# Performance work log

Measured on AMD Instinct MI355X. Metric: run time of the kernel, lower is better.

## Reference

```python
import jax, jax.numpy as jnp
import numpy as np
import math

SCALES = [1, 2, 4, 8]
H = 1024           # hidden_size
NS = len(SCALES)
DS = H // NS       # per-scale dim = 256
NH_S = max(1, 8 // NS)  # heads per scale = 2


def _avg_pool(x, s):
    # x: [B, L, d], kernel=stride=s (L divisible by s)
    B, L, d = x.shape
    return x.reshape(B, L // s, s, d).mean(axis=2)


def _mha(q, k, v, in_w, in_b, out_w, out_b, nh):
    # torch nn.MultiheadAttention, batch_first, no mask.
    d = q.shape[-1]
    wq, wk, wv = in_w[:d], in_w[d:2 * d], in_w[2 * d:]
    bq, bk, bv = in_b[:d], in_b[d:2 * d], in_b[2 * d:]
    qh = q @ wq.T + bq
    kh = k @ wk.T + bk
    vh = v @ wv.T + bv
    B, Lq, _ = qh.shape
    Lk = kh.shape[1]
    hd = d // nh
    qh = qh.reshape(B, Lq, nh, hd).transpose(0, 2, 1, 3)
    kh = kh.reshape(B, Lk, nh, hd).transpose(0, 2, 1, 3)
    vh = vh.reshape(B, Lk, nh, hd).transpose(0, 2, 1, 3)
    scores = jnp.einsum('bhqd,bhkd->bhqk', qh, kh) * (1.0 / math.sqrt(hd))
    w = jax.nn.softmax(scores, axis=-1)
    out = jnp.einsum('bhqk,bhkd->bhqd', w, vh)
    out = out.transpose(0, 2, 1, 3).reshape(B, Lq, d)
    out = out @ out_w.T + out_b
    return out, w.mean(axis=1)  # averaged attn weights (torch default)


def setup_inputs() -> dict:
    key = jax.random.key(0)
    ks = jax.random.split(key, 20)
    B, S = 4, 2048
    f = lambda k, shape: (jax.random.normal(k, shape, dtype=jnp.float32) * 0.02)
    return {
        'query': jax.random.normal(ks[0], (B, S, H), dtype=jnp.float32),
        'key': jax.random.normal(ks[1], (B, S, H), dtype=jnp.float32),
        'value': jax.random.normal(ks[2], (B, S, H), dtype=jnp.float32),
        'wq': f(ks[3], (H, H)), 'bq': f(ks[4], (H,)),
        'wk': f(ks[5], (H, H)), 'bk': f(ks[6], (H,)),
        'wv': f(ks[7], (H, H)), 'bv': f(ks[8], (H,)),
        'mha_in_w': f(ks[9], (NS, 3 * DS, DS)),
        'mha_in_b': f(ks[10], (NS, 3 * DS)),
        'mha_out_w': f(ks[11], (NS, DS, DS)),
        'mha_out_b': f(ks[12], (NS, DS)),
        'fus_w': f(ks[13], (H, H)), 'fus_b': f(ks[14], (H,)),
    }


def reference(query, key, value, wq, bq, wk, bk, wv, bv,
              mha_in_w, mha_in_b, mha_out_w, mha_out_b, fus_w, fus_b):
    q = query @ wq.T + bq
    k = key @ wk.T + bk
    v = value @ wv.T + bv
    outs = []
    weights0 = None
    for i, s in enumerate(SCALES):
        qs = q[..., i * DS:(i + 1) * DS]
        ks_ = k[..., i * DS:(i + 1) * DS]
        vs = v[..., i * DS:(i + 1) * DS]
        if s > 1:
            ks_ = _avg_pool(ks_, s)
            vs = _avg_pool(vs, s)
        attended, w = _mha(qs, ks_, vs, mha_in_w[i], mha_in_b[i],
                           mha_out_w[i], mha_out_b[i], NH_S)
        # F.interpolate back to seq_len is an identity here (query length == seq_len)
        outs.append(attended)
        if i == 0:
            weights0 = w
    fused = jnp.concatenate(outs, axis=-1) @ fus_w.T + fus_b
    return fused, weights0
```

## Files before the change

kernel.cpp:

```cpp
#include <hip/hip_runtime.h>
#include <stdint.h>

typedef unsigned short u16;
typedef __bf16 v8bf __attribute__((ext_vector_type(8)));
typedef float v4f __attribute__((ext_vector_type(4)));
typedef __attribute__((address_space(3))) unsigned lds_t;
typedef const __attribute__((address_space(1))) unsigned g_t;

__device__ __forceinline__ u16 f2bf(float f) {
  union { float f; unsigned u; } v; v.f = f;
  unsigned r = v.u + 0x7FFFu + ((v.u >> 16) & 1u);
  return (u16)(r >> 16);
}
__device__ __forceinline__ float bf2f(u16 h) {
  union { unsigned u; float f; } v; v.u = ((unsigned)h) << 16;
  return v.f;
}
__device__ __forceinline__ ushort4 f4bf(float4 f) {
  ushort4 o;
  o.x = f2bf(f.x); o.y = f2bf(f.y); o.z = f2bf(f.z); o.w = f2bf(f.w);
  return o;
}

__global__ void k_cvt(const float* __restrict__ s, u16* __restrict__ d, long n) {
  long i = ((long)blockIdx.x * blockDim.x + threadIdx.x) * 4;
  long stride = (long)gridDim.x * blockDim.x * 4;
  for (; i < n; i += stride) {
    *(ushort4*)(d + i) = f4bf(*(const float4*)(s + i));
  }
}

__global__ void k_cvtpool(const float* __restrict__ src, u16* __restrict__ dst) {
  int g = blockIdx.x & 255, b = blockIdx.x >> 8;
  int c = threadIdx.x * 4;
  const float* p = src + ((long)b * 2048 + g * 8) * 1024 + c;
  u16* df = dst + ((long)b * 2048 + g * 8) * 1024 + c;
  float4 x[8];
#pragma unroll
  for (int j = 0; j < 8; j++) {
    x[j] = *(const float4*)(p + (long)j * 1024);
    *(ushort4*)(df + (long)j * 1024) = f4bf(x[j]);
  }
  float4 s2[4], s4[2], s8;
#pragma unroll
  for (int j = 0; j < 4; j++) {
    s2[j].x = x[2 * j].x + x[2 * j + 1].x;
    s2[j].y = x[2 * j].y + x[2 * j + 1].y;
    s2[j].z = x[2 * j].z + x[2 * j + 1].z;
    s2[j].w = x[2 * j].w + x[2 * j + 1].w;
  }
#pragma unroll
  for (int j = 0; j < 2; j++) {
    s4[j].x = s2[2 * j].x + s2[2 * j + 1].x;
    s4[j].y = s2[2 * j].y + s2[2 * j + 1].y;
    s4[j].z = s2[2 * j].z + s2[2 * j + 1].z;
    s4[j].w = s2[2 * j].w + s2[2 * j + 1].w;
  }
  s8.x = s4[0].x + s4[1].x; s8.y = s4[0].y + s4[1].y;
  s8.z = s4[0].z + s4[1].z; s8.w = s4[0].w + s4[1].w;
  u16* d2 = dst + ((long)8192 + b * 1024 + g * 4) * 1024 + c;
#pragma unroll
  for (int j = 0; j < 4; j++) {
    float4 t = {s2[j].x * 0.5f, s2[j].y * 0.5f, s2[j].z * 0.5f, s2[j].w * 0.5f};
    *(ushort4*)(d2 + (long)j * 1024) = f4bf(t);
  }
  u16* d4 = dst + ((long)12288 + b * 512 + g * 2) * 1024 + c;
#pragma unroll
  for (int j = 0; j < 2; j++) {
    float4 t = {s4[j].x * 0.25f, s4[j].y * 0.25f, s4[j].z * 0.25f, s4[j].w * 0.25f};
    *(ushort4*)(d4 + (long)j * 1024) = f4bf(t);
  }
  float4 t8 = {s8.x * 0.125f, s8.y * 0.125f, s8.z * 0.125f, s8.w * 0.125f};
  *(ushort4*)(dst + ((long)14336 + b * 256 + g) * 1024 + c) = f4bf(t8);
}

__global__ void k_tc(const float* __restrict__ src, u16* __restrict__ dst, int R, int C) {
  __shared__ float t[32][33];
  long zoff = (long)blockIdx.z * R * C;
  int r0 = blockIdx.y * 32, c0 = blockIdx.x * 32;
  int tx = threadIdx.x & 31, ty = threadIdx.x >> 5;
#pragma unroll
  for (int j = 0; j < 32; j += 8)
    t[ty + j][tx] = src[zoff + (long)(r0 + ty + j) * C + c0 + tx];
  __syncthreads();
#pragma unroll
  for (int j = 0; j < 32; j += 8)
    dst[zoff + (long)(c0 + ty + j) * R + r0 + tx] = f2bf(t[tx][ty + j]);
}

__global__ void k_bcomb_qkv(const float* __restrict__ in_w, const float* __restrict__ in_b,
                            const float* __restrict__ bq, const float* __restrict__ bk,
                            const float* __restrict__ bv, float* __restrict__ out) {
  int gw = (blockIdx.x * 256 + threadIdx.x) >> 6;
  int lane = threadIdx.x & 63;
  int p = gw >> 10, j = gw & 1023, i = j >> 8, of = j & 255;
  const float* bp = p == 0 ? bq : p == 1 ? bk : bv;
  const float* row = in_w + ((long)i * 768 + p * 256 + of) * 256;
  float s = 0.f;
#pragma unroll
  for (int m = 0; m < 4; m++) s += row[lane + m * 64] * bp[i * 256 + lane + m * 64];
#pragma unroll
  for (int m = 32; m >= 1; m >>= 1) s += __shfl_xor(s, m, 64);
  if (lane == 0) out[gw] = in_b[(long)i * 768 + p * 256 + of] + s;
}

__global__ void k_bcomb_f(const float* __restrict__ fw, const float* __restrict__ fb,
                          const float* __restrict__ ob, float* __restrict__ out) {
  int w = (blockIdx.x * 256 + threadIdx.x) >> 6;
  int lane = threadIdx.x & 63;
  const float* row = fw + (long)w * 1024;
  float s = 0.f;
  for (int k = lane; k < 1024; k += 64) s += row[k] * ob[k];
#pragma unroll
  for (int m = 32; m >= 1; m >>= 1) s += __shfl_xor(s, m, 64);
  if (lane == 0) out[w] = fb[w] + s;
}

template<int KS>
__global__ __launch_bounds__(256) void k_ksum(const float* __restrict__ P,
                                              u16* __restrict__ O, long n, int coloff) {
  long i = ((long)blockIdx.x * 256 + threadIdx.x) * 4;
  if (i >= n) return;
  float4 s = *(const float4*)(P + i);
#pragma unroll
  for (int ks = 1; ks < KS; ks++) {
    float4 t = *(const float4*)(P + (long)ks * n + i);
    s.x += t.x; s.y += t.y; s.z += t.z; s.w += t.w;
  }
  *(ushort4*)(O + (i >> 8) * 1024 + coloff + (int)(i & 255)) = f4bf(s);
}

__global__ __launch_bounds__(256) void k_ml0(
    const u16* __restrict__ QHf, const u16* __restrict__ KH,
    float* __restrict__ Mp, float* __restrict__ Lp)
{
  int kc = blockIdx.x;
  int z = blockIdx.z;
  int b = z >> 1, h = z & 1;
  int q0 = blockIdx.y * 64;
  __shared__ u16 KV[2][128][32];
  __shared__ float red[2][4][64];

  const int tid = threadIdx.x, lane = tid & 63, wave = tid >> 6;
  const int q4 = lane >> 4, l16 = lane & 15;
  const int wr = (wave >> 1) * 32, wc = (wave & 1) * 64;
  const int srow = wave * 16 + (lane >> 2), scol = (lane & 3) * 8;
  const float alpha = 0.08838834764831845f;

  v8bf qf[2][4];
#pragma unroll
  for (int mi = 0; mi < 2; mi++)
#pragma unroll
    for (int sub = 0; sub < 4; sub++)
      qf[mi][sub] = *(const v8bf*)(QHf + ((long)b * 2048 + q0 + wr + mi * 16 + l16) * 1024
                                   + h * 128 + sub * 32 + q4 * 8);

  const u16* gK = KH + (long)b * 2048 * 256 + h * 128;
  auto stageK = [&](int buf, int kt, int sub) {
    const u16* g = gK + (long)(kt * 128 + srow) * 256 + sub * 32 + scol;
    __builtin_amdgcn_global_load_lds((g_t*)g, (lds_t*)&KV[buf][wave * 16][0], 16, 0, 0);
    __builtin_amdgcn_global_load_lds((g_t*)(g + 64 * 256), (lds_t*)&KV[buf][64 + wave * 16][0], 16, 0, 0);
  };

  float m_run[2][4], l_run[2][4];
#pragma unroll
  for (int mi = 0; mi < 2; mi++)
#pragma unroll
    for (int i4 = 0; i4 < 4; i4++) { m_run[mi][i4] = -1e30f; l_run[mi][i4] = 0.f; }

  for (int kt = kc * 4; kt < kc * 4 + 4; kt++) {
    v4f s[2][4];
#pragma unroll
    for (int mi = 0; mi < 2; mi++)
#pragma unroll
      for (int ni = 0; ni < 4; ni++) s[mi][ni] = (v4f){0.f, 0.f, 0.f, 0.f};
    stageK(0, kt, 0);
    __syncthreads();
    int cur = 0;
#pragma unroll
    for (int sub = 0; sub < 4; sub++) {
      if (sub < 3) stageK(cur ^ 1, kt, sub + 1);
      v8bf kf[4];
#pragma unroll
      for (int ni = 0; ni < 4; ni++)
        kf[ni] = *(const v8bf*)&KV[cur][wc + ni * 16 + l16][q4 * 8];
#pragma unroll
      for (int mi = 0; mi < 2; mi++)
#pragma unroll
        for (int ni = 0; ni < 4; ni++)
          s[mi][ni] = __builtin_amdgcn_mfma_f32_16x16x32_bf16(qf[mi][sub], kf[ni], s[mi][ni], 0, 0, 0);
      __syncthreads();
      cur ^= 1;
    }
#pragma unroll
    for (int mi = 0; mi < 2; mi++)
#pragma unroll
      for (int ni = 0; ni < 4; ni++) s[mi][ni] *= alpha;
    float mloc[2][4];
#pragma unroll
    for (int mi = 0; mi < 2; mi++)
#pragma unroll
      for (int i4 = 0; i4 < 4; i4++)
        mloc[mi][i4] = fmaxf(fmaxf(s[mi][0][i4], s[mi][1][i4]),
                             fmaxf(s[mi][2][i4], s[mi][3][i4]));
#pragma unroll
    for (int d = 1; d <= 8; d <<= 1)
#pragma unroll
      for (int mi = 0; mi < 2; mi++)
#pragma unroll
        for (int i4 = 0; i4 < 4; i4++)
          mloc[mi][i4] = fmaxf(mloc[mi][i4], __shfl_xor(mloc[mi][i4], d, 64));
    if (l16 == 0) {
#pragma unroll
      for (int mi = 0; mi < 2; mi++)
#pragma unroll
        for (int i4 = 0; i4 < 4; i4++)
          red[0][wave][wr + mi * 16 + q4 * 4 + i4] = mloc[mi][i4];
    }
    __syncthreads();
    float lloc[2][4] = {{0.f, 0.f, 0.f, 0.f}, {0.f, 0.f, 0.f, 0.f}};
#pragma unroll
    for (int mi = 0; mi < 2; mi++)
#pragma unroll
      for (int i4 = 0; i4 < 4; i4++) {
        int rr = wr + mi * 16 + q4 * 4 + i4;
        float mn = fmaxf(fmaxf(red[0][wave][rr], red[0][wave ^ 1][rr]), m_run[mi][i4]);
        float scl = __expf(m_run[mi][i4] - mn);
        m_run[mi][i4] = mn;
        l_run[mi][i4] *= scl;
#pragma unroll
        for (int ni = 0; ni < 4; ni++)
          lloc[mi][i4] += __expf(s[mi][ni][i4] - mn);
      }
#pragma unroll
    for (int d = 1; d <= 8; d <<= 1)
#pragma unroll
      for (int mi = 0; mi < 2; mi++)
#pragma unroll
        for (int i4 = 0; i4 < 4; i4++)
          lloc[mi][i4] += __shfl_xor(lloc[mi][i4], d, 64);
    if (l16 == 0) {
#pragma unroll
      for (int mi = 0; mi < 2; mi++)
#pragma unroll
        for (int i4 = 0; i4 < 4; i4++)
          red[1][wave][wr + mi * 16 + q4 * 4 + i4] = lloc[mi][i4];
    }
    __syncthreads();
#pragma unroll
    for (int mi = 0; mi < 2; mi++)
#pragma unroll
      for (int i4 = 0; i4 < 4; i4++) {
        int rr = wr + mi * 16 + q4 * 4 + i4;
        l_run[mi][i4] += red[1][wave][rr] + red[1][wave ^ 1][rr];
      }
    __syncthreads();
  }

  if ((wave & 1) == 0 && l16 == 0) {
    long zo = ((long)kc * 8 + z) * 2048;
#pragma unroll
    for (int mi = 0; mi < 2; mi++)
#pragma unroll
      for (int i4 = 0; i4 < 4; i4++) {
        int r = q0 + wr + mi * 16 + q4 * 4 + i4;
        Mp[zo + r] = m_run[mi][i4];
        Lp[zo + r] = l_run[mi][i4];
      }
  }
}

__global__ __launch_bounds__(256) void k_mlcomb(
    const float* __restrict__ Mp, const float* __restrict__ Lp,
    float* __restrict__ M0, float* __restrict__ L0)
{
  long r = (long)blockIdx.x * 256 + threadIdx.x;
  float m = -1e30f;
#pragma unroll
  for (int kc = 0; kc < 4; kc++) m = fmaxf(m, Mp[kc * 16384 + r]);
  float l = 0.f;
#pragma unroll
  for (int kc = 0; kc < 4; kc++)
    l += Lp[kc * 16384 + r] * __expf(Mp[kc * 16384 + r] - m);
  M0[r] = m; L0[r] = l;
}

__global__ __launch_bounds__(256) void k_pv0(
    const u16* __restrict__ QHf, const u16* __restrict__ KH,
    const u16* __restrict__ VHT, const float* __restrict__ M0,
    const float* __restrict__ L0, float* __restrict__ PP, float* __restrict__ W0)
{
  int kc = blockIdx.x;
  int b = blockIdx.z;
  int q0 = blockIdx.y * 32;
  __shared__ u16 P[2][32][136];
  __shared__ u16 KV[2][128][32];

  const int tid = threadIdx.x, lane = tid & 63, wave = tid >> 6;
  const int q4 = lane >> 4, l16 = lane & 15;
  const int wr = (wave >> 1) * 16, wc = (wave & 1) * 64;
  const int srow = wave * 16 + (lane >> 2), scol = (lane & 3) * 8;
  const float alpha = 0.08838834764831845f;

  v8bf qf[2][4];
#pragma unroll
  for (int h = 0; h < 2; h++)
#pragma unroll
    for (int sub = 0; sub < 4; sub++)
      qf[h][sub] = *(const v8bf*)(QHf + ((long)b * 2048 + q0 + wr + l16) * 1024
                                  + h * 128 + sub * 32 + q4 * 8);
  float mv[2][4], il[2][4];
#pragma unroll
  for (int h = 0; h < 2; h++)
#pragma unroll
    for (int i4 = 0; i4 < 4; i4++) {
      long r = (long)(b * 2 + h) * 2048 + q0 + wr + q4 * 4 + i4;
      mv[h][i4] = M0[r];
      il[h][i4] = 1.0f / L0[r];
    }

  const u16* gK = KH + (long)b * 2048 * 256;
  auto stageK = [&](int buf, int h, int kt, int sub) {
    const u16* g = gK + (long)(kt * 128 + srow) * 256 + h * 128 + sub * 32 + scol;
    __builtin_amdgcn_global_load_lds((g_t*)g, (lds_t*)&KV[buf][wave * 16][0], 16, 0, 0);
    __builtin_amdgcn_global_load_lds((g_t*)(g + 64 * 256), (lds_t*)&KV[buf][64 + wave * 16][0], 16, 0, 0);
  };
  auto stageV = [&](int buf, int h, int kt, int sub) {
    const u16* g = VHT + ((long)(b * 2 + h) * 128 + srow) * 2048 + kt * 128 + sub * 32 + scol;
    __builtin_amdgcn_global_load_lds((g_t*)g, (lds_t*)&KV[buf][wave * 16][0], 16, 0, 0);
    __builtin_amdgcn_global_load_lds((g_t*)(g + (long)64 * 2048), (lds_t*)&KV[buf][64 + wave * 16][0], 16, 0, 0);
  };

  v4f acc[2][4];
#pragma unroll
  for (int h = 0; h < 2; h++)
#pragma unroll
    for (int ni = 0; ni < 4; ni++) acc[h][ni] = (v4f){0.f, 0.f, 0.f, 0.f};

  for (int kt = kc * 4; kt < kc * 4 + 4; kt++) {
    float p0[4][4];
#pragma unroll
    for (int h = 0; h < 2; h++) {
      v4f s[4];
#pragma unroll
      for (int ni = 0; ni < 4; ni++) s[ni] = (v4f){0.f, 0.f, 0.f, 0.f};
      stageK(0, h, kt, 0);
      __syncthreads();
      int cur = 0;
#pragma unroll
      for (int sub = 0; sub < 4; sub++) {
        if (sub < 3) stageK(cur ^ 1, h, kt, sub + 1);
        v8bf kf[4];
#pragma unroll
        for (int ni = 0; ni < 4; ni++)
          kf[ni] = *(const v8bf*)&KV[cur][wc + ni * 16 + l16][q4 * 8];
#pragma unroll
        for (int ni = 0; ni < 4; ni++)
          s[ni] = __builtin_amdgcn_mfma_f32_16x16x32_bf16(qf[h][sub], kf[ni], s[ni], 0, 0, 0);
        __syncthreads();
        cur ^= 1;
      }
#pragma unroll
      for (int ni = 0; ni < 4; ni++)
#pragma unroll
        for (int i4 = 0; i4 < 4; i4++) {
          float p = __expf(s[ni][i4] * alpha - mv[h][i4]) * il[h][i4];
          P[h][wr + q4 * 4 + i4][wc + ni * 16 + l16] = f2bf(p);
          if (h == 0) p0[ni][i4] = p;
          else {
            W0[((long)b * 2048 + q0 + wr + q4 * 4 + i4) * 2048
               + kt * 128 + wc + ni * 16 + l16] = 0.5f * (p0[ni][i4] + p);
          }
        }
    }
#pragma unroll
    for (int h = 0; h < 2; h++) {
      stageV(0, h, kt, 0);
      __syncthreads();
      int cv = 0;
#pragma unroll
      for (int sub = 0; sub < 4; sub++) {
        if (sub < 3) stageV(cv ^ 1, h, kt, sub + 1);
        v8bf pf = *(const v8bf*)&P[h][wr + l16][sub * 32 + q4 * 8];
        v8bf vf[4];
#pragma unroll
        for (int ni = 0; ni < 4; ni++)
          vf[ni] = *(const v8bf*)&KV[cv][wc + ni * 16 + l16][q4 * 8];
#pragma unroll
        for (int ni = 0; ni < 4; ni++)
          acc[h][ni] = __builtin_amdgcn_mfma_f32_16x16x32_bf16(pf, vf[ni], acc[h][ni], 0, 0, 0);
        __syncthreads();
        cv ^= 1;
      }
    }
  }

  float* pp = PP + ((long)kc * 8192 + (long)b * 2048) * 256;
#pragma unroll
  for (int h = 0; h < 2; h++)
#pragma unroll
    for (int ni = 0; ni < 4; ni++)
#pragma unroll
      for (int i4 = 0; i4 < 4; i4++) {
        int r = q0 + wr + q4 * 4 + i4;
        int c = wc + ni * 16 + l16;
        pp[(long)r * 256 + h * 128 + c] = acc[h][ni][i4];
      }
}

__global__ __launch_bounds__(256) void k_flash(
    const u16* __restrict__ QHf, const u16* __restrict__ KH,
    const u16* __restrict__ VHT, u16* __restrict__ AOf)
{
  int z = blockIdx.z;
  int i = (z >> 3) + 1;
  int b = (z >> 1) & 3, h = z & 1;
  int Ls = 2048 >> i;
  int nkt = Ls >> 7;
  long ro = (long)(16384 - (8192 >> (i - 1))) * 256;
  int q0 = blockIdx.y * 64;

  __shared__ u16 QP[64][136];
  __shared__ u16 KV[2][128][32];
  __shared__ float red[2][4][64];

  const int tid = threadIdx.x, lane = tid & 63, wave = tid >> 6;
  const int q4 = lane >> 4, l16 = lane & 15;
  const int wr = (wave >> 1) * 32, wc = (wave & 1) * 64;
  const int srow = wave * 16 + (lane >> 2);
  const int scol = (lane & 3) * 8;

  {
    const u16* gq = QHf + ((long)b * 2048 + q0) * 1024 + i * 256 + h * 128;
    int idx = tid * 4;
#pragma unroll
    for (int j = 0; j < 4; j++) {
      int r = (idx + j) >> 4, ch = (idx + j) & 15;
      *(ulonglong2*)&QP[r][ch * 8] = *(const ulonglong2*)(gq + (long)r * 1024 + ch * 8);
    }
  }
  __syncthreads();
  v8bf qf[2][4];
#pragma unroll
  for (int mi = 0; mi < 2; mi++)
#pragma unroll
    for (int sub = 0; sub < 4; sub++)
      qf[mi][sub] = *(const v8bf*)&QP[wr + mi * 16 + l16][sub * 32 + q4 * 8];
  __syncthreads();

  const u16* gK = KH + ro + (long)b * Ls * 256 + h * 128;
  const u16* gV = VHT + ro + (long)(b * 2 + h) * 128 * Ls;

  auto stageK = [&](int buf, int kt, int sub) {
    const u16* g = gK + (long)(kt * 128 + srow) * 256 + sub * 32 + scol;
    __builtin_amdgcn_global_load_lds((g_t*)g, (lds_t*)&KV[buf][wave * 16][0], 16, 0, 0);
    __builtin_amdgcn_global_load_lds((g_t*)(g + 64 * 256), (lds_t*)&KV[buf][64 + wave * 16][0], 16, 0, 0);
  };
  auto stageV = [&](int buf, int kt, int sub) {
    const u16* g = gV + (long)srow * Ls + kt * 128 + sub * 32 + scol;
    __builtin_amdgcn_global_load_lds((g_t*)g, (lds_t*)&KV[buf][wave * 16][0], 16, 0, 0);
    __builtin_amdgcn_global_load_lds((g_t*)(g + (long)64 * Ls), (lds_t*)&KV[buf][64 + wave * 16][0], 16, 0, 0);
  };

  v4f acc_o[2][4];
  float m_run[2][4], l_run[2][4];
#pragma unroll
  for (int mi = 0; mi < 2; mi++)
#pragma unroll
    for (int ni = 0; ni < 4; ni++) acc_o[mi][ni] = (v4f){0.f, 0.f, 0.f, 0.f};
#pragma unroll
  for (int mi = 0; mi < 2; mi++)
#pragma unroll
    for (int i4 = 0; i4 < 4; i4++) { m_run[mi][i4] = -1e30f; l_run[mi][i4] = 0.f; }

  const float alpha = 0.08838834764831845f;

  for (int kt = 0; kt < nkt; kt++) {
    v4f s[2][4];
#pragma unroll
    for (int mi = 0; mi < 2; mi++)
#pragma unroll
      for (int ni = 0; ni < 4; ni++) s[mi][ni] = (v4f){0.f, 0.f, 0.f, 0.f};
    stageK(0, kt, 0);
    __syncthreads();
    int cur = 0;
#pragma unroll
    for (int sub = 0; sub < 4; sub++) {
      if (sub < 3) stageK(cur ^ 1, kt, sub + 1);
      v8bf kf[4];
#pragma unroll
      for (int ni = 0; ni < 4; ni++)
        kf[ni] = *(const v8bf*)&KV[cur][wc + ni * 16 + l16][q4 * 8];
#pragma unroll
      for (int mi = 0; mi < 2; mi++)
#pragma unroll
        for (int ni = 0; ni < 4; ni++)
          s[mi][ni] = __builtin_amdgcn_mfma_f32_16x16x32_bf16(qf[mi][sub], kf[ni], s[mi][ni], 0, 0, 0);
      __syncthreads();
      cur ^= 1;
    }
    stageV(0, kt, 0);

#pragma unroll
    for (int mi = 0; mi < 2; mi++)
#pragma unroll
      for (int ni = 0; ni < 4; ni++) s[mi][ni] *= alpha;
    float mloc[2][4];
#pragma unroll
    for (int mi = 0; mi < 2; mi++)
#pragma unroll
      for (int i4 = 0; i4 < 4; i4++)
        mloc[mi][i4] = fmaxf(fmaxf(s[mi][0][i4], s[mi][1][i4]),
                             fmaxf(s[mi][2][i4], s[mi][3][i4]));
#pragma unroll
    for (int d = 1; d <= 8; d <<= 1)
#pragma unroll
      for (int mi = 0; mi < 2; mi++)
#pragma unroll
        for (int i4 = 0; i4 < 4; i4++)
          mloc[mi][i4] = fmaxf(mloc[mi][i4], __shfl_xor(mloc[mi][i4], d, 64));
    if (l16 == 0) {
#pragma unroll
      for (int mi = 0; mi < 2; mi++)
#pragma unroll
        for (int i4 = 0; i4 < 4; i4++)
          red[0][wave][wr + mi * 16 + q4 * 4 + i4] = mloc[mi][i4];
    }
    __syncthreads();
    float scl[2][4];
#pragma unroll
    for (int mi = 0; mi < 2; mi++)
#pragma unroll
      for (int i4 = 0; i4 < 4; i4++) {
        int rr = wr + mi * 16 + q4 * 4 + i4;
        float mn = fmaxf(fmaxf(red[0][wave][rr], red[0][wave ^ 1][rr]), m_run[mi][i4]);
        scl[mi][i4] = __expf(m_run[mi][i4] - mn);
        m_run[mi][i4] = mn;
      }
    float lloc[2][4] = {{0.f, 0.f, 0.f, 0.f}, {0.f, 0.f, 0.f, 0.f}};
#pragma unroll
    for (int mi = 0; mi < 2; mi++)
#pragma unroll
      for (int ni = 0; ni < 4; ni++)
#pragma unroll
        for (int i4 = 0; i4 < 4; i4++) {
          float p = __expf(s[mi][ni][i4] - m_run[mi][i4]);
          lloc[mi][i4] += p;
          QP[wr + mi * 16 + q4 * 4 + i4][wc + ni * 16 + l16] = f2bf(p);
        }
#pragma unroll
    for (int d = 1; d <= 8; d <<= 1)
#pragma unroll
      for (int mi = 0; mi < 2; mi++)
#pragma unroll
        for (int i4 = 0; i4 < 4; i4++)
          lloc[mi][i4] += __shfl_xor(lloc[mi][i4], d, 64);
    if (l16 == 0) {
#pragma unroll
      for (int mi = 0; mi < 2; mi++)
#pragma unroll
        for (int i4 = 0; i4 < 4; i4++)
          red[1][wave][wr + mi * 16 + q4 * 4 + i4] = lloc[mi][i4];
    }
#pragma unroll
    for (int mi = 0; mi < 2; mi++)
#pragma unroll
      for (int ni = 0; ni < 4; ni++)
#pragma unroll
        for (int i4 = 0; i4 < 4; i4++) acc_o[mi][ni][i4] *= scl[mi][i4];
    __syncthreads();
#pragma unroll
    for (int mi = 0; mi < 2; mi++)
#pragma unroll
      for (int i4 = 0; i4 < 4; i4++) {
        int rr = wr + mi * 16 + q4 * 4 + i4;
        l_run[mi][i4] = l_run[mi][i4] * scl[mi][i4] + red[1][wave][rr] + red[1][wave ^ 1][rr];
      }

    int cv = 0;
#pragma unroll
    for (int sub = 0; sub < 4; sub++) {
      if (sub < 3) stageV(cv ^ 1, kt, sub + 1);
      v8bf pf[2], vf[4];
#pragma unroll
      for (int mi = 0; mi < 2; mi++)
        pf[mi] = *(const v8bf*)&QP[wr + mi * 16 + l16][sub * 32 + q4 * 8];
#pragma unroll
      for (int ni = 0; ni < 4; ni++)
        vf[ni] = *(const v8bf*)&KV[cv][wc + ni * 16 + l16][q4 * 8];
#pragma unroll
      for (int mi = 0; mi < 2; mi++)
#pragma unroll
        for (int ni = 0; ni < 4; ni++)
          acc_o[mi][ni] = __builtin_amdgcn_mfma_f32_16x16x32_bf16(pf[mi], vf[ni], acc_o[mi][ni], 0, 0, 0);
      __syncthreads();
      cv ^= 1;
    }
  }

#pragma unroll
  for (int mi = 0; mi < 2; mi++)
#pragma unroll
    for (int i4 = 0; i4 < 4; i4++) {
      float inv = 1.0f / l_run[mi][i4];
#pragma unroll
      for (int ni = 0; ni < 4; ni++) {
        int r = q0 + wr + mi * 16 + q4 * 4 + i4;
        int c = wc + ni * 16 + l16;
        AOf[((long)b * 2048 + r) * 1024 + i * 256 + h * 128 + c] =
            f2bf(acc_o[mi][ni][i4] * inv);
      }
    }
}

template<int WBF>
__global__ __launch_bounds__(256) void k_gemm(
    const u16* __restrict__ A, long ldA, long sA1, long sA2,
    const u16* __restrict__ B, long ldB, long sB1, long sB2,
    void* __restrict__ Cv, long ldC, long sC1, long sC2, long sCk,
    const float* __restrict__ bias, long sBias, float alpha,
    int M, int N, int K, int nz2, int KS)
{
  __shared__ u16 As[2][128][32];
  __shared__ u16 Bs[2][128][32];
  int z = blockIdx.z;
  int ks = z % KS; int zz = z / KS;
  int z1 = zz / nz2, z2 = zz - z1 * nz2;
  A += (long)z1 * sA1 + (long)z2 * sA2 + (long)ks * K;
  B += (long)z1 * sB1 + (long)z2 * sB2 + (long)ks * K;
  long coff = (long)z1 * sC1 + (long)z2 * sC2 + (long)ks * sCk;
  const float* bz = bias ? bias + (long)z2 * sBias : nullptr;
  const int m0 = blockIdx.y * 128, n0 = blockIdx.x * 128;
  const int tid = threadIdx.x;
  const int lane = tid & 63;
  const int wave = tid >> 6;
  const int wr = (wave >> 1) * 64, wc = (wave & 1) * 64;
  const int q4 = lane >> 4, l16 = lane & 15;

  const int srow = wave * 16 + (lane >> 2);
  const int scol = (lane & 3) * 8;
  const u16* gA = A + (long)(m0 + srow) * ldA + scol;
  const u16* gB = B + (long)(n0 + srow) * ldB + scol;

  auto stage = [&](int buf, int kt) {
    __builtin_amdgcn_global_load_lds((g_t*)(gA + kt), (lds_t*)&As[buf][wave * 16][0], 16, 0, 0);
    __builtin_amdgcn_global_load_lds((g_t*)(gA + 64 * ldA + kt), (lds_t*)&As[buf][64 + wave * 16][0], 16, 0, 0);
    __builtin_amdgcn_global_load_lds((g_t*)(gB + kt), (lds_t*)&Bs[buf][wave * 16][0], 16, 0, 0);
    __builtin_amdgcn_global_load_lds((g_t*)(gB + 64 * ldB + kt), (lds_t*)&Bs[buf][64 + wave * 16][0], 16, 0, 0);
  };

  v4f acc[4][4];
#pragma unroll
  for (int i = 0; i < 4; i++)
#pragma unroll
    for (int j = 0; j < 4; j++) acc[i][j] = (v4f){0.f, 0.f, 0.f, 0.f};

  stage(0, 0);
  __syncthreads();
  int cur = 0;
  for (int kt = 0; kt < K; kt += 32) {
    if (kt + 32 < K) stage(cur ^ 1, kt + 32);
    v8bf af[4], bf[4];
#pragma unroll
    for (int i = 0; i < 4; i++) af[i] = *(const v8bf*)&As[cur][wr + i * 16 + l16][q4 * 8];
#pragma unroll
    for (int i = 0; i < 4; i++) bf[i] = *(const v8bf*)&Bs[cur][wc + i * 16 + l16][q4 * 8];
#pragma unroll
    for (int mi = 0; mi < 4; mi++)
#pragma unroll
      for (int ni = 0; ni < 4; ni++)
        acc[mi][ni] = __builtin_amdgcn_mfma_f32_16x16x32_bf16(af[mi], bf[ni], acc[mi][ni], 0, 0, 0);
    __syncthreads();
    cur ^= 1;
  }

#pragma unroll
  for (int mi = 0; mi < 4; mi++) {
    int rb = m0 + wr + mi * 16 + q4 * 4;
#pragma unroll
    for (int ni = 0; ni < 4; ni++) {
      int c = n0 + wc + ni * 16 + l16;
      float bv = bz ? bz[c] : 0.f;
#pragma unroll
      for (int i = 0; i < 4; i++) {
        int r = rb + i;
        float val = acc[mi][ni][i] * alpha + bv;
        if (WBF) ((u16*)Cv)[coff + (long)r * ldC + c] = f2bf(val);
        else     ((float*)Cv)[coff + (long)r * ldC + c] = val;
      }
    }
  }
}

__global__ __launch_bounds__(256) void k_gemm_kv(
    const u16* __restrict__ Xk, const u16* __restrict__ Xv,
    const u16* __restrict__ WCkv, const float* __restrict__ Bckv,
    u16* __restrict__ KH, u16* __restrict__ VHT)
{
  __shared__ u16 As[2][128][32];
  __shared__ u16 Bs[2][128][32];
  const int isV = blockIdx.z;
  const int m0 = blockIdx.y * 128, n0 = blockIdx.x * 128;
  const int scale = m0 < 8192 ? 0 : (m0 < 12288 ? 1 : (m0 < 14336 ? 2 : 3));
  const int rbase = scale == 0 ? 0 : (scale == 1 ? 8192 : (scale == 2 ? 12288 : 14336));
  const int lsh = 11 - scale;
  const u16* A = isV ? Xv : Xk;
  const u16* B = WCkv + (long)isV * 1048576 + (long)scale * 262144;
  const float* bz = Bckv + isV * 1024 + scale * 256;

  const int tid = threadIdx.x;
  const int lane = tid & 63, wave = tid >> 6;
  const int wr = (wave >> 1) * 64, wc = (wave & 1) * 64;
  const int q4 = lane >> 4, l16 = lane & 15;
  const int srow = wave * 16 + (lane >> 2);
  const int scol = (lane & 3) * 8;
  const u16* gA = A + (long)(m0 + srow) * 1024 + scol;
  const u16* gB = B + (long)(n0 + srow) * 1024 + scol;

  auto stage = [&](int buf, int kt) {
    __builtin_amdgcn_global_load_lds((g_t*)(gA + kt), (lds_t*)&As[buf][wave * 16][0], 16, 0, 0);
    __builtin_amdgcn_global_load_lds((g_t*)(gA + 64 * 1024 + kt), (lds_t*)&As[buf][64 + wave * 16][0], 16, 0, 0);
    __builtin_amdgcn_global_load_lds((g_t*)(gB + kt), (lds_t*)&Bs[buf][wave * 16][0], 16, 0, 0);
    __builtin_amdgcn_global_load_lds((g_t*)(gB + 64 * 1024 + kt), (lds_t*)&Bs[buf][64 + wave * 16][0], 16, 0, 0);
  };

  v4f acc[4][4];
#pragma unroll
  for (int i = 0; i < 4; i++)
#pragma unroll
    for (int j = 0; j < 4; j++) acc[i][j] = (v4f){0.f, 0.f, 0.f, 0.f};

  stage(0, 0);
  __syncthreads();
  int cur = 0;
  for (int kt = 0; kt < 1024; kt += 32) {
    if (kt + 32 < 1024) stage(cur ^ 1, kt + 32);
    v8bf af[4], bf[4];
#pragma unroll
    for (int i = 0; i < 4; i++) af[i] = *(const v8bf*)&As[cur][wr + i * 16 + l16][q4 * 8];
#pragma unroll
    for (int i = 0; i < 4; i++) bf[i] = *(const v8bf*)&Bs[cur][wc + i * 16 + l16][q4 * 8];
#pragma unroll
    for (int mi = 0; mi < 4; mi++)
#pragma unroll
      for (int ni = 0; ni < 4; ni++)
        acc[mi][ni] = __builtin_amdgcn_mfma_f32_16x16x32_bf16(af[mi], bf[ni], acc[mi][ni], 0, 0, 0);
    __syncthreads();
    cur ^= 1;
  }

#pragma unroll
  for (int mi = 0; mi < 4; mi++) {
    int rb = m0 + wr + mi * 16 + q4 * 4;
#pragma unroll
    for (int ni = 0; ni < 4; ni++) {
      int c = n0 + wc + ni * 16 + l16;
      float bv = bz[c];
#pragma unroll
      for (int i = 0; i < 4; i++) {
        int r = rb + i;
        float val = acc[mi][ni][i] + bv;
        if (!isV) {
          KH[(long)r * 256 + c] = f2bf(val);
        } else {
          int rl = r - rbase;
          int b = rl >> lsh, t = rl & ((1 << lsh) - 1);
          int h = c >> 7, n = c & 127;
          VHT[(long)rbase * 256 + (((long)(b * 2 + h) * 128 + n) << lsh) + t] = f2bf(val);
        }
      }
    }
  }
}

extern "C" void kernel_launch(void* const* d_in, const int* in_sizes, int n_in,
                              void* d_out, int out_size, void* d_ws, size_t ws_size,
                              hipStream_t stream) {
  const float* query = (const float*)d_in[0];
  const float* key_  = (const float*)d_in[1];
  const float* value = (const float*)d_in[2];
  const float* wq    = (const float*)d_in[3];
  const float* bq    = (const float*)d_in[4];
  const float* wk    = (const float*)d_in[5];
  const float* bk    = (const float*)d_in[6];
  const float* wv    = (const float*)d_in[7];
  const float* bv    = (const float*)d_in[8];
  const float* in_w  = (const float*)d_in[9];
  const float* in_b  = (const float*)d_in[10];
  const float* out_w = (const float*)d_in[11];
  const float* out_b = (const float*)d_in[12];
  const float* fus_w = (const float*)d_in[13];
  const float* fus_b = (const float*)d_in[14];
  (void)in_sizes; (void)n_in; (void)out_size; (void)ws_size;

  float* outF  = (float*)d_out;
  float* outW0 = outF + (long)4 * 2048 * 1024;

  char* base = (char*)d_ws;
  size_t off = 0;
  auto alloc = [&](size_t bytes) -> void* {
    void* p = base + off;
    off = (off + bytes + 255) & ~(size_t)255;
    return p;
  };
  const long NX = (long)8192 * 1024;
  u16* Winb = (u16*)alloc((size_t)4 * 768 * 256 * 2);
  u16* Wfb  = (u16*)alloc((size_t)1024 * 1024 * 2);
  u16* WoT  = (u16*)alloc((size_t)4 * 256 * 256 * 2);
  u16* WT   = (u16*)alloc((size_t)3 * 1024 * 1024 * 2);
  u16* WC   = (u16*)alloc((size_t)3 * 1024 * 1024 * 2);
  u16* WFc  = (u16*)alloc((size_t)1024 * 1024 * 2);
  float* Bc  = (float*)alloc((size_t)3 * 1024 * 4);
  float* fbc = (float*)alloc((size_t)1024 * 4);
  u16* Xq    = (u16*)alloc((size_t)NX * 2);
  u16* XkAll = (u16*)alloc((size_t)15360 * 1024 * 2);
  u16* XvAll = (u16*)alloc((size_t)15360 * 1024 * 2);
  u16* QHf = (u16*)alloc((size_t)8192 * 1024 * 2);
  u16* KH  = (u16*)alloc((size_t)15360 * 256 * 2);
  u16* VHT = (u16*)alloc((size_t)15360 * 256 * 2);
  float* M0 = (float*)alloc((size_t)8 * 2048 * 4);
  float* L0 = (float*)alloc((size_t)8 * 2048 * 4);
  float* Mp = (float*)alloc((size_t)4 * 8 * 2048 * 4);
  float* Lp = (float*)alloc((size_t)4 * 8 * 2048 * 4);
  float* PP = (float*)alloc((size_t)4 * 8192 * 256 * 4);
  u16* AOf = (u16*)alloc((size_t)8192 * 1024 * 2);

  const long AOsz = (long)8192 * 256;

  k_cvt<<<1024, 256, 0, stream>>>(query, Xq, NX);
  k_cvtpool<<<1024, 256, 0, stream>>>(key_,  XkAll);
  k_cvtpool<<<1024, 256, 0, stream>>>(value, XvAll);
  k_cvt<<<192, 256, 0, stream>>>(in_w, Winb, 4 * 768 * 256);
  k_cvt<<<256, 256, 0, stream>>>(fus_w, Wfb, 1024 * 1024);
  k_tc<<<dim3(32, 32, 1), 256, 0, stream>>>(wq, WT, 1024, 1024);
  k_tc<<<dim3(32, 32, 1), 256, 0, stream>>>(wk, WT + (long)1024 * 1024, 1024, 1024);
  k_tc<<<dim3(32, 32, 1), 256, 0, stream>>>(wv, WT + (long)2 * 1024 * 1024, 1024, 1024);
  k_tc<<<dim3(8, 8, 4), 256, 0, stream>>>(out_w, WoT, 256, 256);
  k_bcomb_qkv<<<768, 256, 0, stream>>>(in_w, in_b, bq, bk, bv, Bc);
  k_bcomb_f<<<256, 256, 0, stream>>>(fus_w, fus_b, out_b, fbc);

  k_gemm<1><<<dim3(8, 2, 12), 256, 0, stream>>>(
      Winb, 256, 65536, 196608,
      WT, 1024, 1048576, 256,
      WC, 1024, 1048576, 262144, 0,
      nullptr, 0, 1.f, 256, 1024, 256, 4, 1);
  k_gemm<1><<<dim3(2, 8, 4), 256, 0, stream>>>(
      Wfb, 1024, 0, 256,
      WoT, 256, 0, 65536,
      WFc, 1024, 0, 256, 0,
      nullptr, 0, 1.f, 1024, 256, 256, 4, 1);

  k_gemm<1><<<dim3(8, 64, 1), 256, 0, stream>>>(
      Xq, 1024, 0, 0, WC, 1024, 0, 0,
      QHf, 1024, 0, 0, 0, Bc, 0, 1.f, 8192, 1024, 1024, 1, 1);
  k_gemm_kv<<<dim3(2, 120, 2), 256, 0, stream>>>(
      XkAll, XvAll, WC + (long)1024 * 1024, Bc + 1024, KH, VHT);

  k_ml0<<<dim3(4, 32, 8), 256, 0, stream>>>(QHf, KH, Mp, Lp);
  k_mlcomb<<<64, 256, 0, stream>>>(Mp, Lp, M0, L0);
  k_pv0<<<dim3(4, 64, 4), 256, 0, stream>>>(QHf, KH, VHT, M0, L0, PP, outW0);
  k_ksum<4><<<2048, 256, 0, stream>>>(PP, AOf, AOsz, 0);

  k_flash<<<dim3(1, 32, 24), 256, 0, stream>>>(QHf, KH, VHT, AOf);

  k_gemm<0><<<dim3(8, 64, 1), 256, 0, stream>>>(
      AOf, 1024, 0, 0, WFc, 1024, 0, 0,
      outF, 1024, 0, 0, 0, fbc, 0, 1.f, 8192, 1024, 1024, 1, 1);
}
```

Before: 518.8 us.

## Split scale-0 attention into eight key chunks and interleave both heads per stage

The scale-0 kernels (row-stats and PV/weights) now split the 2048 keys into 8 chunks instead of 4, doubling the grid to improve occupancy. The combine and ksum reductions and the partial buffers are resized to match. k_pv0 is also restructured to process both heads together in each sub-step: K/V for both heads are staged into a doubled LDS buffer, which halves the number of barriers. Q fragments are now reloaded from global memory per sub-step instead of being kept in registers. The split adds more partial-sum traffic through PP and the ksum reduction.

```diff
diff --git a/kernel.cpp b/kernel.cpp
--- a/kernel.cpp
+++ b/kernel.cpp
@@ -168,7 +168,7 @@
 #pragma unroll
     for (int i4 = 0; i4 < 4; i4++) { m_run[mi][i4] = -1e30f; l_run[mi][i4] = 0.f; }
 
-  for (int kt = kc * 4; kt < kc * 4 + 4; kt++) {
+  for (int kt = kc * 2; kt < kc * 2 + 2; kt++) {
     v4f s[2][4];
 #pragma unroll
     for (int mi = 0; mi < 2; mi++)
@@ -277,10 +277,10 @@
   long r = (long)blockIdx.x * 256 + threadIdx.x;
   float m = -1e30f;
 #pragma unroll
-  for (int kc = 0; kc < 4; kc++) m = fmaxf(m, Mp[kc * 16384 + r]);
+  for (int kc = 0; kc < 8; kc++) m = fmaxf(m, Mp[kc * 16384 + r]);
   float l = 0.f;
 #pragma unroll
-  for (int kc = 0; kc < 4; kc++)
+  for (int kc = 0; kc < 8; kc++)
     l += Lp[kc * 16384 + r] * __expf(Mp[kc * 16384 + r] - m);
   M0[r] = m; L0[r] = l;
 }
@@ -294,7 +294,7 @@
   int b = blockIdx.z;
   int q0 = blockIdx.y * 32;
   __shared__ u16 P[2][32][136];
-  __shared__ u16 KV[2][128][32];
+  __shared__ u16 KV[2][2][128][32];
 
   const int tid = threadIdx.x, lane = tid & 63, wave = tid >> 6;
   const int q4 = lane >> 4, l16 = lane & 15;
@@ -302,13 +302,6 @@
   const int srow = wave * 16 + (lane >> 2), scol = (lane & 3) * 8;
   const float alpha = 0.08838834764831845f;
 
-  v8bf qf[2][4];
-#pragma unroll
-  for (int h = 0; h < 2; h++)
-#pragma unroll
-    for (int sub = 0; sub < 4; sub++)
-      qf[h][sub] = *(const v8bf*)(QHf + ((long)b * 2048 + q0 + wr + l16) * 1024
-                                  + h * 128 + sub * 32 + q4 * 8);
   float mv[2][4], il[2][4];
 #pragma unroll
   for (int h = 0; h < 2; h++)
@@ -320,15 +313,23 @@
     }
 
   const u16* gK = KH + (long)b * 2048 * 256;
-  auto stageK = [&](int buf, int h, int kt, int sub) {
-    const u16* g = gK + (long)(kt * 128 + srow) * 256 + h * 128 + sub * 32 + scol;
-    __builtin_amdgcn_global_load_lds((g_t*)g, (lds_t*)&KV[buf][wave * 16][0], 16, 0, 0);
-    __builtin_amdgcn_global_load_lds((g_t*)(g + 64 * 256), (lds_t*)&KV[buf][64 + wave * 16][0], 16, 0, 0);
+  const u16* gQ = QHf + ((long)b * 2048 + q0 + wr + l16) * 1024;
+
+  auto stageK2 = [&](int buf, int kt, int sub) {
+#pragma unroll
+    for (int h = 0; h < 2; h++) {
+      const u16* g = gK + (long)(kt * 128 + srow) * 256 + h * 128 + sub * 32 + scol;
+      __builtin_amdgcn_global_load_lds((g_t*)g, (lds_t*)&KV[buf][h][wave * 16][0], 16, 0, 0);
+      __builtin_amdgcn_global_load_lds((g_t*)(g + 64 * 256), (lds_t*)&KV[buf][h][64 + wave * 16][0], 16, 0, 0);
+    }
   };
-  auto stageV = [&](int buf, int h, int kt, int sub) {
-    const u16* g = VHT + ((long)(b * 2 + h) * 128 + srow) * 2048 + kt * 128 + sub * 32 + scol;
-    __builtin_amdgcn_global_load_lds((g_t*)g, (lds_t*)&KV[buf][wave * 16][0], 16, 0, 0);
-    __builtin_amdgcn_global_load_lds((g_t*)(g + (long)64 * 2048), (lds_t*)&KV[buf][64 + wave * 16][0], 16, 0, 0);
+  auto stageV2 = [&](int buf, int kt, int sub) {
+#pragma unroll
+    for (int h = 0; h < 2; h++) {
+      const u16* g = VHT + ((long)(b * 2 + h) * 128 + srow) * 2048 + kt * 128 + sub * 32 + scol;
+      __builtin_amdgcn_global_load_lds((g_t*)g, (lds_t*)&KV[buf][h][wave * 16][0], 16, 0, 0);
+      __builtin_amdgcn_global_load_lds((g_t*)(g + (long)64 * 2048), (lds_t*)&KV[buf][h][64 + wave * 16][0], 16, 0, 0);
+    }
   };
 
   v4f acc[2][4];
@@ -337,61 +338,68 @@
 #pragma unroll
     for (int ni = 0; ni < 4; ni++) acc[h][ni] = (v4f){0.f, 0.f, 0.f, 0.f};
 
-  for (int kt = kc * 4; kt < kc * 4 + 4; kt++) {
-    float p0[4][4];
-#pragma unroll
-    for (int h = 0; h < 2; h++) {
-      v4f s[4];
-#pragma unroll
-      for (int ni = 0; ni < 4; ni++) s[ni] = (v4f){0.f, 0.f, 0.f, 0.f};
-      stageK(0, h, kt, 0);
+  for (int kt = kc * 2; kt < kc * 2 + 2; kt++) {
+    v4f s[2][4];
+#pragma unroll
+    for (int h = 0; h < 2; h++)
+#pragma unroll
+      for (int ni = 0; ni < 4; ni++) s[h][ni] = (v4f){0.f, 0.f, 0.f, 0.f};
+    stageK2(0, kt, 0);
+    __syncthreads();
+    int cur = 0;
+#pragma unroll
+    for (int sub = 0; sub < 4; sub++) {
+      if (sub < 3) stageK2(cur ^ 1, kt, sub + 1);
+      v8bf q2[2], kf[2][4];
+#pragma unroll
+      for (int h = 0; h < 2; h++)
+        q2[h] = *(const v8bf*)(gQ + h * 128 + sub * 32 + q4 * 8);
+#pragma unroll
+      for (int h = 0; h < 2; h++)
+#pragma unroll
+        for (int ni = 0; ni < 4; ni++)
+          kf[h][ni] = *(const v8bf*)&KV[cur][h][wc + ni * 16 + l16][q4 * 8];
+#pragma unroll
+      for (int h = 0; h < 2; h++)
+#pragma unroll
+        for (int ni = 0; ni < 4; ni++)
+          s[h][ni] = __builtin_amdgcn_mfma_f32_16x16x32_bf16(q2[h], kf[h][ni], s[h][ni], 0, 0, 0);
       __syncthreads();
-      int cur = 0;
-#pragma unroll
-      for (int sub = 0; sub < 4; sub++) {
-        if (sub < 3) stageK(cur ^ 1, h, kt, sub + 1);
-        v8bf kf[4];
+      cur ^= 1;
+    }
+#pragma unroll
+    for (int ni = 0; ni < 4; ni++)
+#pragma unroll
+      for (int i4 = 0; i4 < 4; i4++) {
+        float p0 = __expf(s[0][ni][i4] * alpha - mv[0][i4]) * il[0][i4];
+        float p1 = __expf(s[1][ni][i4] * alpha - mv[1][i4]) * il[1][i4];
+        int rr = wr + q4 * 4 + i4, cc = wc + ni * 16 + l16;
+        P[0][rr][cc] = f2bf(p0);
+        P[1][rr][cc] = f2bf(p1);
+        W0[((long)b * 2048 + q0 + rr) * 2048 + kt * 128 + cc] = 0.5f * (p0 + p1);
+      }
+    stageV2(0, kt, 0);
+    __syncthreads();
+    int cv = 0;
+#pragma unroll
+    for (int sub = 0; sub < 4; sub++) {
+      if (sub < 3) stageV2(cv ^ 1, kt, sub + 1);
+      v8bf pf[2], vf[2][4];
+#pragma unroll
+      for (int h = 0; h < 2; h++)
+        pf[h] = *(const v8bf*)&P[h][wr + l16][sub * 32 + q4 * 8];
+#pragma unroll
+      for (int h = 0; h < 2; h++)
 #pragma unroll
         for (int ni = 0; ni < 4; ni++)
-          kf[ni] = *(const v8bf*)&KV[cur][wc + ni * 16 + l16][q4 * 8];
+          vf[h][ni] = *(const v8bf*)&KV[cv][h][wc + ni * 16 + l16][q4 * 8];
+#pragma unroll
+      for (int h = 0; h < 2; h++)
 #pragma unroll
         for (int ni = 0; ni < 4; ni++)
-          s[ni] = __builtin_amdgcn_mfma_f32_16x16x32_bf16(qf[h][sub], kf[ni], s[ni], 0, 0, 0);
-        __syncthreads();
-        cur ^= 1;
-      }
-#pragma unroll
-      for (int ni = 0; ni < 4; ni++)
-#pragma unroll
-        for (int i4 = 0; i4 < 4; i4++) {
-          float p = __expf(s[ni][i4] * alpha - mv[h][i4]) * il[h][i4];
-          P[h][wr + q4 * 4 + i4][wc + ni * 16 + l16] = f2bf(p);
-          if (h == 0) p0[ni][i4] = p;
-          else {
-            W0[((long)b * 2048 + q0 + wr + q4 * 4 + i4) * 2048
-               + kt * 128 + wc + ni * 16 + l16] = 0.5f * (p0[ni][i4] + p);
-          }
-        }
-    }
-#pragma unroll
-    for (int h = 0; h < 2; h++) {
-      stageV(0, h, kt, 0);
+          acc[h][ni] = __builtin_amdgcn_mfma_f32_16x16x32_bf16(pf[h], vf[h][ni], acc[h][ni], 0, 0, 0);
       __syncthreads();
-      int cv = 0;
-#pragma unroll
-      for (int sub = 0; sub < 4; sub++) {
-        if (sub < 3) stageV(cv ^ 1, h, kt, sub + 1);
-        v8bf pf = *(const v8bf*)&P[h][wr + l16][sub * 32 + q4 * 8];
-        v8bf vf[4];
-#pragma unroll
-        for (int ni = 0; ni < 4; ni++)
-          vf[ni] = *(const v8bf*)&KV[cv][wc + ni * 16 + l16][q4 * 8];
-#pragma unroll
-        for (int ni = 0; ni < 4; ni++)
-          acc[h][ni] = __builtin_amdgcn_mfma_f32_16x16x32_bf16(pf, vf[ni], acc[h][ni], 0, 0, 0);
-        __syncthreads();
-        cv ^= 1;
-      }
+      cv ^= 1;
     }
   }
 
@@ -820,9 +828,9 @@
   u16* VHT = (u16*)alloc((size_t)15360 * 256 * 2);
   float* M0 = (float*)alloc((size_t)8 * 2048 * 4);
   float* L0 = (float*)alloc((size_t)8 * 2048 * 4);
-  float* Mp = (float*)alloc((size_t)4 * 8 * 2048 * 4);
-  float* Lp = (float*)alloc((size_t)4 * 8 * 2048 * 4);
-  float* PP = (float*)alloc((size_t)4 * 8192 * 256 * 4);
+  float* Mp = (float*)alloc((size_t)8 * 8 * 2048 * 4);
+  float* Lp = (float*)alloc((size_t)8 * 8 * 2048 * 4);
+  float* PP = (float*)alloc((size_t)8 * 8192 * 256 * 4);
   u16* AOf = (u16*)alloc((size_t)8192 * 1024 * 2);
 
   const long AOsz = (long)8192 * 256;
@@ -856,10 +864,10 @@
   k_gemm_kv<<<dim3(2, 120, 2), 256, 0, stream>>>(
       XkAll, XvAll, WC + (long)1024 * 1024, Bc + 1024, KH, VHT);
 
-  k_ml0<<<dim3(4, 32, 8), 256, 0, stream>>>(QHf, KH, Mp, Lp);
+  k_ml0<<<dim3(8, 32, 8), 256, 0, stream>>>(QHf, KH, Mp, Lp);
   k_mlcomb<<<64, 256, 0, stream>>>(Mp, Lp, M0, L0);
-  k_pv0<<<dim3(4, 64, 4), 256, 0, stream>>>(QHf, KH, VHT, M0, L0, PP, outW0);
-  k_ksum<4><<<2048, 256, 0, stream>>>(PP, AOf, AOsz, 0);
+  k_pv0<<<dim3(8, 64, 4), 256, 0, stream>>>(QHf, KH, VHT, M0, L0, PP, outW0);
+  k_ksum<8><<<2048, 256, 0, stream>>>(PP, AOf, AOsz, 0);
 
   k_flash<<<dim3(1, 32, 24), 256, 0, stream>>>(QHf, KH, VHT, AOf);
 
```

After: 524.2 us. Within noise of the previous version (+1.0%).
